# Kernel tuning notes

Hardware: AMD Instinct MI355X
Metric: run time of the kernel (lower is better)

The kernel has to match this reference:

```python
import jax, jax.numpy as jnp
import numpy as np

N = 50000   # nodes
E = 800000  # edges per layer
D = 128     # feature dim
H = 256     # mlp hidden
O = 3       # output dim


def setup_inputs() -> dict:
    key = jax.random.key(0)
    ks = jax.random.split(key, 16)
    def lin(k, fan_out, fan_in):
        s = 1.0 / np.sqrt(fan_in)
        kw, kb = jax.random.split(k)
        return (jax.random.uniform(kw, (fan_out, fan_in), jnp.float32, -s, s),
                jax.random.uniform(kb, (fan_out,), jnp.float32, -s, s))
    x = jax.random.normal(ks[0], (N, D), jnp.float32)
    edge_idx0 = jax.random.randint(ks[1], (2, E), 0, N, dtype=jnp.int64)
    edge_idx1 = jax.random.randint(ks[2], (2, E), 0, N, dtype=jnp.int64)
    Wl1, bl1 = lin(ks[3], D, D)   # SAGE layer1: lin_l (aggregated neighbors, with bias)
    Wr1, _ = lin(ks[4], D, D)     # SAGE layer1: lin_r (root, no bias)
    Wl2, bl2 = lin(ks[5], D, D)
    Wr2, _ = lin(ks[6], D, D)
    Ws, bs = lin(ks[7], D, D)     # skip_fc
    W1, b1 = lin(ks[8], H, D)     # mlp hidden
    W2, b2 = lin(ks[9], O, H)     # mlp out
    return dict(x=x, edge_idx0=edge_idx0, edge_idx1=edge_idx1,
                Wl1=Wl1, bl1=bl1, Wr1=Wr1, Wl2=Wl2, bl2=bl2, Wr2=Wr2,
                Ws=Ws, bs=bs, W1=W1, b1=b1, W2=W2, b2=b2)


def _sage(x, ei, Wl, bl, Wr):
    # PyG SAGEConv with mean aggregation: out = lin_l(mean_j x_j) + lin_r(x_i)
    src, dst = ei[0], ei[1]
    agg = jax.ops.segment_sum(x[src], dst, num_segments=N)          # [N, D] gather-scatter
    cnt = jax.ops.segment_sum(jnp.ones((ei.shape[1],), x.dtype), dst, num_segments=N)
    agg = agg / jnp.maximum(cnt, 1.0)[:, None]
    return agg @ Wl.T + bl + x @ Wr.T


def reference(x, edge_idx0, edge_idx1, Wl1, bl1, Wr1, Wl2, bl2, Wr2,
              Ws, bs, W1, b1, W2, b2):
    inp = x
    h = _sage(x, edge_idx0, Wl1, bl1, Wr1)
    h = _sage(h, edge_idx1, Wl2, bl2, Wr2)
    h = h + (inp @ Ws.T + bs)            # skip connection
    h = jax.nn.relu(h @ W1.T + b1)       # MLP head
    return h @ W2.T + b2                  # [N, 3]
```

## Files before the change

kernel.cpp:

```cpp
#include <hip/hip_runtime.h>
#include <hip/hip_bf16.h>


#define DD 128
#define SB 8
#define CH 4096
typedef unsigned short u16;
typedef __attribute__((ext_vector_type(8))) short short8;
typedef __attribute__((ext_vector_type(4))) float f32x4;

__device__ inline u16 f2bf(float f) {
    __hip_bfloat16 h = __float2bfloat16(f);
    u16 u;
    __builtin_memcpy(&u, &h, 2);
    return u;
}
__device__ inline unsigned pack2(float lo, float hi) {
    return (unsigned)f2bf(lo) | ((unsigned)f2bf(hi) << 16);
}
__device__ inline float bf_lo(unsigned u) { union { unsigned x; float f; } c; c.x = u << 16; return c.f; }
__device__ inline float bf_hi(unsigned u) { union { unsigned x; float f; } c; c.x = u & 0xffff0000u; return c.f; }

struct CastJobs {
    const float4* src[6];
    uint2* dst[6];
    int qstart[7];
};
__global__ __launch_bounds__(256) void cast_kernel(CastJobs jb) {
    int q = blockIdx.x * 256 + threadIdx.x;
    if (q >= jb.qstart[6]) return;
    int i = 0;
#pragma unroll
    for (int k = 1; k < 6; ++k) if (q >= jb.qstart[k]) i = k;
    int local = q - jb.qstart[i];
    float4 v = jb.src[i][local];
    jb.dst[i][local] = make_uint2(pack2(v.x, v.y), pack2(v.z, v.w));
}

__global__ __launch_bounds__(256) void hist1_kernel(const int* __restrict__ dst0, int* __restrict__ h0,
                                                    const int* __restrict__ dst1, int* __restrict__ h1,
                                                    int e0, int e1, int nb, int P) {
    int arr = blockIdx.y;
    const int* dst = arr ? dst1 : dst0;
    int* hist = arr ? h1 : h0;
    int e = arr ? e1 : e0;
    __shared__ int h[256];
    int t = threadIdx.x;
    h[t] = 0;
    __syncthreads();
    int base = blockIdx.x * CH;
    int hi = min(base + CH, e);
    for (int i = base + t; i < hi; i += 256) atomicAdd(&h[dst[i] >> SB], 1);
    __syncthreads();
    if (t < nb) hist[t * P + blockIdx.x] = h[t];
}

__global__ __launch_bounds__(256) void bscan_kernel(const int* __restrict__ h0, int* __restrict__ bb0, int* __restrict__ rp0, int e0,
                                                    const int* __restrict__ h1, int* __restrict__ bb1, int* __restrict__ rp1, int e1,
                                                    int nb, int P, int n) {
    int arr = blockIdx.x;
    const int* hist = arr ? h1 : h0;
    int* bb = arr ? bb1 : bb0;
    int* rp = arr ? rp1 : rp0;
    int E = arr ? e1 : e0;
    __shared__ int s[256];
    int t = threadIdx.x;
    int v = 0;
    if (t < nb) {
        const int* row = hist + (size_t)t * P;
        for (int p = 0; p < P; ++p) v += row[p];
    }
    s[t] = v;
    __syncthreads();
    for (int off = 1; off < 256; off <<= 1) {
        int u = (t >= off) ? s[t - off] : 0;
        __syncthreads();
        s[t] += u;
        __syncthreads();
    }
    if (t < nb) bb[t] = s[t] - v;
    if (t == 0) { bb[nb] = E; rp[n] = E; }
}

__global__ __launch_bounds__(256) void offs_kernel(int* __restrict__ h0, const int* __restrict__ bb0,
                                                   int* __restrict__ h1, const int* __restrict__ bb1,
                                                   int P) {
    int arr = blockIdx.y;
    int* hist = arr ? h1 : h0;
    const int* bb = arr ? bb1 : bb0;
    int b = blockIdx.x;
    __shared__ int s[256];
    int t = threadIdx.x;
    int v = (t < P) ? hist[b * P + t] : 0;
    s[t] = v;
    __syncthreads();
    for (int off = 1; off < 256; off <<= 1) {
        int u = (t >= off) ? s[t - off] : 0;
        __syncthreads();
        s[t] += u;
        __syncthreads();
    }
    if (t < P) hist[b * P + t] = s[t] - v + bb[b];
}

__global__ __launch_bounds__(256) void scatter1_kernel(
    const int* __restrict__ src0, const int* __restrict__ dst0, const int* __restrict__ h0, unsigned* __restrict__ binned0,
    const int* __restrict__ src1, const int* __restrict__ dst1, const int* __restrict__ h1, unsigned* __restrict__ binned1,
    int e0, int e1, int nb, int P) {
    int arr = blockIdx.y;
    const int* src = arr ? src1 : src0;
    const int* dst = arr ? dst1 : dst0;
    const int* hist = arr ? h1 : h0;
    unsigned* binned = arr ? binned1 : binned0;
    int e = arr ? e1 : e0;
    int p = blockIdx.x;
    __shared__ int cnt[256];
    int t = threadIdx.x;
    if (t < nb) cnt[t] = hist[t * P + p];
    __syncthreads();
    int base = p * CH;
    int hi = min(base + CH, e);
    for (int i = base + t; i < hi; i += 256) {
        int d = dst[i];
        int pos = atomicAdd(&cnt[d >> SB], 1);
        binned[pos] = ((unsigned)d << 16) | (unsigned)src[i];
    }
}

__global__ __launch_bounds__(256) void place_kernel(
    const unsigned* __restrict__ binned0, const int* __restrict__ bb0, int* __restrict__ rp0, u16* __restrict__ csr0,
    const unsigned* __restrict__ binned1, const int* __restrict__ bb1, int* __restrict__ rp1, u16* __restrict__ csr1,
    int n, int nb) {
    int arr = blockIdx.y;
    const unsigned* binned = arr ? binned1 : binned0;
    const int* bb = arr ? bb1 : bb0;
    int* rp = arr ? rp1 : rp0;
    u16* csr = arr ? csr1 : csr0;
    int b = blockIdx.x;
    __shared__ int cnt[256];
    __shared__ int s[256];
    int t = threadIdx.x;
    int base = bb[b], end = bb[b + 1];
    cnt[t] = 0;
    __syncthreads();
    for (int i = base + t; i < end; i += 256)
        atomicAdd(&cnt[(binned[i] >> 16) & 255], 1);
    __syncthreads();
    int deg = cnt[t];
    s[t] = deg;
    __syncthreads();
    for (int off = 1; off < 256; off <<= 1) {
        int u = (t >= off) ? s[t - off] : 0;
        __syncthreads();
        s[t] += u;
        __syncthreads();
    }
    int gpos = base + s[t] - deg;
    int node = (b << SB) + t;
    if (node < n) rp[node] = gpos;
    cnt[t] = gpos;
    __syncthreads();
    for (int i = base + t; i < end; i += 256) {
        unsigned pk = binned[i];
        int ld = (pk >> 16) & 255;
        int pos = atomicAdd(&cnt[ld], 1);
        csr[pos] = (u16)(pk & 0xffffu);
    }
}

__global__ __launch_bounds__(256) void agg1_kernel(const u16* __restrict__ G1,
                                                   const u16* __restrict__ csr,
                                                   const int* __restrict__ rp,
                                                   const float* __restrict__ bl1,
                                                   u16* __restrict__ h1, int n) {
    int g = (blockIdx.x * 256 + threadIdx.x) >> 4;
    int lane = threadIdx.x & 15;
    if (g >= n) return;
    int start = rp[g], end = rp[g + 1];
    int d = end - start;
    const uint4* X4 = (const uint4*)G1;
    float acc[8] = {0.f, 0.f, 0.f, 0.f, 0.f, 0.f, 0.f, 0.f};
    int e = start;
    for (; e + 1 < end; e += 2) {
        int s0 = csr[e], s1 = csr[e + 1];
        uint4 v0 = X4[(size_t)s0 * 48 + lane];
        uint4 v1 = X4[(size_t)s1 * 48 + lane];
        acc[0] += bf_lo(v0.x) + bf_lo(v1.x); acc[1] += bf_hi(v0.x) + bf_hi(v1.x);
        acc[2] += bf_lo(v0.y) + bf_lo(v1.y); acc[3] += bf_hi(v0.y) + bf_hi(v1.y);
        acc[4] += bf_lo(v0.z) + bf_lo(v1.z); acc[5] += bf_hi(v0.z) + bf_hi(v1.z);
        acc[6] += bf_lo(v0.w) + bf_lo(v1.w); acc[7] += bf_hi(v0.w) + bf_hi(v1.w);
    }
    if (e < end) {
        int s0 = csr[e];
        uint4 v0 = X4[(size_t)s0 * 48 + lane];
        acc[0] += bf_lo(v0.x); acc[1] += bf_hi(v0.x);
        acc[2] += bf_lo(v0.y); acc[3] += bf_hi(v0.y);
        acc[4] += bf_lo(v0.z); acc[5] += bf_hi(v0.z);
        acc[6] += bf_lo(v0.w); acc[7] += bf_hi(v0.w);
    }
    float sc = 1.0f / (float)max(d, 1);
    uint4 m = X4[(size_t)g * 48 + 16 + lane];
    const float4* bl = (const float4*)bl1;
    float4 ba = bl[lane * 2], bb = bl[lane * 2 + 1];
    uint4 r;
    r.x = pack2(acc[0] * sc + bf_lo(m.x) + ba.x, acc[1] * sc + bf_hi(m.x) + ba.y);
    r.y = pack2(acc[2] * sc + bf_lo(m.y) + ba.z, acc[3] * sc + bf_hi(m.y) + ba.w);
    r.z = pack2(acc[4] * sc + bf_lo(m.z) + bb.x, acc[5] * sc + bf_hi(m.z) + bb.y);
    r.w = pack2(acc[6] * sc + bf_lo(m.w) + bb.z, acc[7] * sc + bf_hi(m.w) + bb.w);
    ((uint4*)h1)[(size_t)g * 16 + lane] = r;
}

__global__ __launch_bounds__(256) void agg2_kernel(const u16* __restrict__ G2,
                                                   const u16* __restrict__ G1,
                                                   const u16* __restrict__ csr,
                                                   const int* __restrict__ rp,
                                                   const float* __restrict__ bl2,
                                                   const float* __restrict__ bs,
                                                   u16* __restrict__ h3, int n) {
    int g = (blockIdx.x * 256 + threadIdx.x) >> 4;
    int lane = threadIdx.x & 15;
    if (g >= n) return;
    int start = rp[g], end = rp[g + 1];
    int d = end - start;
    const uint4* X4 = (const uint4*)G2;
    float acc[8] = {0.f, 0.f, 0.f, 0.f, 0.f, 0.f, 0.f, 0.f};
    int e = start;
    for (; e + 1 < end; e += 2) {
        int s0 = csr[e], s1 = csr[e + 1];
        uint4 v0 = X4[(size_t)s0 * 32 + lane];
        uint4 v1 = X4[(size_t)s1 * 32 + lane];
        acc[0] += bf_lo(v0.x) + bf_lo(v1.x); acc[1] += bf_hi(v0.x) + bf_hi(v1.x);
        acc[2] += bf_lo(v0.y) + bf_lo(v1.y); acc[3] += bf_hi(v0.y) + bf_hi(v1.y);
        acc[4] += bf_lo(v0.z) + bf_lo(v1.z); acc[5] += bf_hi(v0.z) + bf_hi(v1.z);
        acc[6] += bf_lo(v0.w) + bf_lo(v1.w); acc[7] += bf_hi(v0.w) + bf_hi(v1.w);
    }
    if (e < end) {
        int s0 = csr[e];
        uint4 v0 = X4[(size_t)s0 * 32 + lane];
        acc[0] += bf_lo(v0.x); acc[1] += bf_hi(v0.x);
        acc[2] += bf_lo(v0.y); acc[3] += bf_hi(v0.y);
        acc[4] += bf_lo(v0.z); acc[5] += bf_hi(v0.z);
        acc[6] += bf_lo(v0.w); acc[7] += bf_hi(v0.w);
    }
    float sc = 1.0f / (float)max(d, 1);
    uint4 m2 = X4[(size_t)g * 32 + 16 + lane];
    uint4 m1 = ((const uint4*)G1)[(size_t)g * 48 + 32 + lane];
    const float4* c2 = (const float4*)bl2;
    const float4* cs = (const float4*)bs;
    float4 ba = c2[lane * 2], bb = c2[lane * 2 + 1];
    float4 sa = cs[lane * 2], sb = cs[lane * 2 + 1];
    uint4 r;
    r.x = pack2(acc[0] * sc + bf_lo(m2.x) + bf_lo(m1.x) + ba.x + sa.x,
                acc[1] * sc + bf_hi(m2.x) + bf_hi(m1.x) + ba.y + sa.y);
    r.y = pack2(acc[2] * sc + bf_lo(m2.y) + bf_lo(m1.y) + ba.z + sa.z,
                acc[3] * sc + bf_hi(m2.y) + bf_hi(m1.y) + ba.w + sa.w);
    r.z = pack2(acc[4] * sc + bf_lo(m2.z) + bf_lo(m1.z) + bb.x + sb.x,
                acc[5] * sc + bf_hi(m2.z) + bf_hi(m1.z) + bb.y + sb.y);
    r.w = pack2(acc[6] * sc + bf_lo(m2.w) + bf_lo(m1.w) + bb.z + sb.z,
                acc[7] * sc + bf_hi(m2.w) + bf_hi(m1.w) + bb.w + sb.w);
    ((uint4*)h3)[(size_t)g * 16 + lane] = r;
}

template <bool F32A>
__global__ __launch_bounds__(256) void mfma_gemm(const void* __restrict__ Av,
                                                 const u16* __restrict__ W,
                                                 const float* __restrict__ bias,
                                                 u16* __restrict__ C, int M, int NC, int mB) {
    __shared__ u16 As[64 * 136];
    __shared__ u16 Bs[128 * 136];
    const int t = threadIdx.x;
    const int rowBase = (blockIdx.x % mB) * 64;
    const int colBase = (blockIdx.x / mB) * 128;
    const int w = t >> 6, lane = t & 63, r = lane & 15, half = lane >> 4;

    f32x4 acc[8];
#pragma unroll
    for (int i = 0; i < 8; ++i) acc[i] = (f32x4){0.f, 0.f, 0.f, 0.f};

#pragma unroll
    for (int i = 0; i < 4; ++i) {
        int id = t + 256 * i, row = id >> 4, cc = id & 15;
        int gr = rowBase + row;
        uint4 v = make_uint4(0u, 0u, 0u, 0u);
        if (gr < M) {
            if (F32A) {
                const float* A = (const float*)Av;
                float4 a = *(const float4*)&A[(size_t)gr * DD + cc * 8];
                float4 b = *(const float4*)&A[(size_t)gr * DD + cc * 8 + 4];
                v = make_uint4(pack2(a.x, a.y), pack2(a.z, a.w), pack2(b.x, b.y), pack2(b.z, b.w));
            } else {
                v = ((const uint4*)Av)[(size_t)gr * 16 + cc];
            }
        }
        *(uint4*)&As[row * 136 + cc * 8] = v;
    }
#pragma unroll
    for (int i = 0; i < 8; ++i) {
        int id = t + 256 * i, row = id >> 4, cc = id & 15;
        *(uint4*)&Bs[row * 136 + cc * 8] = ((const uint4*)W)[(size_t)(colBase + row) * 16 + cc];
    }
    __syncthreads();
    const u16* aB = &As[(w * 16 + r) * 136 + half * 8];
    const u16* bB = &Bs[r * 136 + half * 8];
#pragma unroll
    for (int kk = 0; kk < 4; ++kk) {
        short8 af = *(const short8*)(aB + kk * 32);
#pragma unroll
        for (int ct = 0; ct < 8; ++ct) {
            short8 bf = *(const short8*)(bB + ct * (16 * 136) + kk * 32);
            acc[ct] = __builtin_amdgcn_mfma_f32_16x16x32_bf16(af, bf, acc[ct], 0, 0, 0);
        }
    }

#pragma unroll
    for (int ct = 0; ct < 8; ++ct) {
        int col = colBase + ct * 16 + r;
        float bv = bias ? bias[col] : 0.f;
#pragma unroll
        for (int reg = 0; reg < 4; ++reg) {
            int row = rowBase + w * 16 + half * 4 + reg;
            if (row < M) C[(size_t)row * NC + col] = f2bf(acc[ct][reg] + bv);
        }
    }
}

__global__ __launch_bounds__(256) void gemm_out_kernel(const u16* __restrict__ h3,
                                                       const u16* __restrict__ W1,
                                                       const float* __restrict__ b1,
                                                       const float* __restrict__ W2,
                                                       const float* __restrict__ b2,
                                                       float* __restrict__ out, int M) {
    __shared__ u16 As[64 * 136];
    __shared__ u16 Bs[128 * 136];
    __shared__ float w2s[3 * 256];
    __shared__ float b1s[256];
    const int t = threadIdx.x;
    const int rowBase = blockIdx.x * 64;
    const int w = t >> 6, lane = t & 63, r = lane & 15, half = lane >> 4;

    for (int i = t; i < 768; i += 256) w2s[i] = W2[i];
    b1s[t] = b1[t];
#pragma unroll
    for (int i = 0; i < 4; ++i) {
        int id = t + 256 * i, row = id >> 4, cc = id & 15;
        int gr = rowBase + row;
        uint4 v = make_uint4(0u, 0u, 0u, 0u);
        if (gr < M) v = ((const uint4*)h3)[(size_t)gr * 16 + cc];
        *(uint4*)&As[row * 136 + cc * 8] = v;
    }

    f32x4 acc[2][8];
#pragma unroll
    for (int ch = 0; ch < 2; ++ch)
#pragma unroll
        for (int i = 0; i < 8; ++i) acc[ch][i] = (f32x4){0.f, 0.f, 0.f, 0.f};

    for (int ch = 0; ch < 2; ++ch) {
        __syncthreads();
        if (ch) {
        }
#pragma unroll
        for (int i = 0; i < 8; ++i) {
            int id = t + 256 * i, row = id >> 4, cc = id & 15;
            *(uint4*)&Bs[row * 136 + cc * 8] = ((const uint4*)W1)[(size_t)(ch * 128 + row) * 16 + cc];
        }
        __syncthreads();
        const u16* aB = &As[(w * 16 + r) * 136 + half * 8];
        const u16* bB = &Bs[r * 136 + half * 8];
#pragma unroll
        for (int kk = 0; kk < 4; ++kk) {
            short8 af = *(const short8*)(aB + kk * 32);
#pragma unroll
            for (int ct = 0; ct < 8; ++ct) {
                short8 bf = *(const short8*)(bB + ct * (16 * 136) + kk * 32);
                acc[ch][ct] = __builtin_amdgcn_mfma_f32_16x16x32_bf16(af, bf, acc[ch][ct], 0, 0, 0);
            }
        }
    }

    float p[4][3] = {{0.f}};
#pragma unroll
    for (int ch = 0; ch < 2; ++ch) {
#pragma unroll
        for (int ct = 0; ct < 8; ++ct) {
            int col = ch * 128 + ct * 16 + r;
            float bv = b1s[col];
            float w0 = w2s[0 * 256 + col], w1 = w2s[1 * 256 + col], w2v = w2s[2 * 256 + col];
#pragma unroll
            for (int reg = 0; reg < 4; ++reg) {
                float h4 = fmaxf(acc[ch][ct][reg] + bv, 0.f);
                p[reg][0] += h4 * w0;
                p[reg][1] += h4 * w1;
                p[reg][2] += h4 * w2v;
            }
        }
    }
#pragma unroll
    for (int m = 1; m < 16; m <<= 1)
#pragma unroll
        for (int reg = 0; reg < 4; ++reg)
#pragma unroll
            for (int o = 0; o < 3; ++o) p[reg][o] += __shfl_xor(p[reg][o], m);
    if (r == 0) {
#pragma unroll
        for (int reg = 0; reg < 4; ++reg) {
            int row = rowBase + w * 16 + half * 4 + reg;
            if (row < M) {
                out[(size_t)row * 3 + 0] = p[reg][0] + b2[0];
                out[(size_t)row * 3 + 1] = p[reg][1] + b2[1];
                out[(size_t)row * 3 + 2] = p[reg][2] + b2[2];
            }
        }
    }
}

extern "C" void kernel_launch(void* const* d_in, const int* in_sizes, int n_in,
                              void* d_out, int out_size, void* d_ws, size_t ws_size,
                              hipStream_t stream) {
    const float* x   = (const float*)d_in[0];
    const int*   ei0 = (const int*)d_in[1];
    const int*   ei1 = (const int*)d_in[2];
    const float* Wl1 = (const float*)d_in[3];
    const float* bl1 = (const float*)d_in[4];
    const float* Wr1 = (const float*)d_in[5];
    const float* Wl2 = (const float*)d_in[6];
    const float* bl2 = (const float*)d_in[7];
    const float* Wr2 = (const float*)d_in[8];
    const float* Wsk = (const float*)d_in[9];
    const float* bsk = (const float*)d_in[10];
    const float* W1  = (const float*)d_in[11];
    const float* b1  = (const float*)d_in[12];
    const float* W2  = (const float*)d_in[13];
    const float* b2  = (const float*)d_in[14];
    float* out = (float*)d_out;

    const int N  = in_sizes[0] / DD;
    const int E0 = in_sizes[1] / 2;
    const int E1 = in_sizes[2] / 2;
    const int H  = in_sizes[12];

    const int* src0 = ei0;      const int* dst0 = ei0 + E0;
    const int* src1 = ei1;      const int* dst1 = ei1 + E1;

    const int nb   = (N + 255) >> SB;
    const int Emax = (E0 > E1) ? E0 : E1;
    const int P    = (Emax + CH - 1) / CH;

    char* wp = (char*)d_ws;
    auto carve = [&](size_t bytes) { char* p = wp; wp += (bytes + 255) & ~(size_t)255; return p; };
    u16* G1   = (u16*)carve((size_t)N * 384 * 2);
    u16* G2   = (u16*)carve((size_t)N * 256 * 2);
    u16* h1h  = (u16*)carve((size_t)N * DD * 2);
    u16* h3h  = (u16*)carve((size_t)N * DD * 2);
    u16* wc1  = (u16*)carve((size_t)384 * DD * 2);
    u16* wc2  = (u16*)carve((size_t)256 * DD * 2);
    u16* w1h  = (u16*)carve((size_t)H * DD * 2);
    int* rp0  = (int*)carve((size_t)(N + 1) * 4);
    int* rp1  = (int*)carve((size_t)(N + 1) * 4);
    u16* csr0 = (u16*)carve((size_t)E0 * 2);
    u16* csr1 = (u16*)carve((size_t)E1 * 2);
    unsigned* binned0 = (unsigned*)carve((size_t)E0 * 4);
    unsigned* binned1 = (unsigned*)carve((size_t)E1 * 4);
    int* hist1_0 = (int*)carve((size_t)nb * P * 4);
    int* hist1_1 = (int*)carve((size_t)nb * P * 4);
    int* bb0 = (int*)carve((size_t)(nb + 1) * 4);
    int* bb1 = (int*)carve((size_t)(nb + 1) * 4);

    CastJobs jb;
    const float* srcs[6] = {Wl1, Wr1, Wsk, Wl2, Wr2, W1};
    u16* dsts[6] = {wc1, wc1 + 128 * DD, wc1 + 256 * DD, wc2, wc2 + 128 * DD, w1h};
    int  cnts[6] = {DD * DD, DD * DD, DD * DD, DD * DD, DD * DD, H * DD};
    int q = 0;
    for (int i = 0; i < 6; ++i) {
        jb.src[i] = (const float4*)srcs[i];
        jb.dst[i] = (uint2*)dsts[i];
        jb.qstart[i] = q;
        q += cnts[i] / 4;
    }
    jb.qstart[6] = q;

    const int gAgg = (N * 16 + 255) / 256;
    const int mB   = (N + 63) / 64;

    cast_kernel<<<(q + 255) / 256, 256, 0, stream>>>(jb);
    hist1_kernel<<<dim3(P, 2), 256, 0, stream>>>(dst0, hist1_0, dst1, hist1_1, E0, E1, nb, P);
    bscan_kernel<<<2, 256, 0, stream>>>(hist1_0, bb0, rp0, E0, hist1_1, bb1, rp1, E1, nb, P, N);
    offs_kernel<<<dim3(nb, 2), 256, 0, stream>>>(hist1_0, bb0, hist1_1, bb1, P);
    scatter1_kernel<<<dim3(P, 2), 256, 0, stream>>>(src0, dst0, hist1_0, binned0,
                                                    src1, dst1, hist1_1, binned1, E0, E1, nb, P);
    place_kernel<<<dim3(nb, 2), 256, 0, stream>>>(binned0, bb0, rp0, csr0,
                                                  binned1, bb1, rp1, csr1, N, nb);

    mfma_gemm<true><<<mB * 3, 256, 0, stream>>>(x, wc1, nullptr, G1, N, 384, mB);
    agg1_kernel<<<gAgg, 256, 0, stream>>>(G1, csr0, rp0, bl1, h1h, N);
    mfma_gemm<false><<<mB * 2, 256, 0, stream>>>(h1h, wc2, nullptr, G2, N, 256, mB);
    agg2_kernel<<<gAgg, 256, 0, stream>>>(G2, G1, csr1, rp1, bl2, bsk, h3h, N);
    gemm_out_kernel<<<mB, 256, 0, stream>>>(h3h, w1h, b1, W2, b2, out, N);
}
```

Before: 294.2 us.

## Persistent MFMA GEMMs with preswizzled weights, parallel histogram rowsum, deeper gather unroll

The GEMMs become persistent kernels. Each block loads its weight slice once into LDS in an MFMA-friendly swizzled layout, and each wave loops over 16-row tiles, reading A directly from global memory into registers instead of staging it through LDS. The output GEMM keeps all 256 hidden columns in registers per tile, which removes its two-chunk reload. The single-block serial histogram row sum is split into a parallel rowsum kernel, and the aggregation loops unroll to four gathers per step for more memory-level parallelism. The code assumes M is divisible by 16 since bounds checks were dropped, and it uses more registers.

```diff
diff --git a/kernel.cpp b/kernel.cpp
--- a/kernel.cpp
+++ b/kernel.cpp
@@ -55,21 +55,35 @@
     if (t < nb) hist[t * P + blockIdx.x] = h[t];
 }
 
-__global__ __launch_bounds__(256) void bscan_kernel(const int* __restrict__ h0, int* __restrict__ bb0, int* __restrict__ rp0, int e0,
-                                                    const int* __restrict__ h1, int* __restrict__ bb1, int* __restrict__ rp1, int e1,
-                                                    int nb, int P, int n) {
+__global__ __launch_bounds__(256) void rowsum_kernel(const int* __restrict__ h0, int* __restrict__ bs0,
+                                                     const int* __restrict__ h1, int* __restrict__ bs1,
+                                                     int P) {
+    int arr = blockIdx.y;
+    const int* hist = arr ? h1 : h0;
+    int* bs = arr ? bs1 : bs0;
+    int b = blockIdx.x;
+    __shared__ int s[256];
+    int t = threadIdx.x;
+    s[t] = (t < P) ? hist[b * P + t] : 0;
+    __syncthreads();
+    for (int off = 128; off; off >>= 1) {
+        if (t < off) s[t] += s[t + off];
+        __syncthreads();
+    }
+    if (t == 0) bs[b] = s[0];
+}
+
+__global__ __launch_bounds__(256) void bscan_kernel(const int* __restrict__ bs0, int* __restrict__ bb0, int* __restrict__ rp0, int e0,
+                                                    const int* __restrict__ bs1, int* __restrict__ bb1, int* __restrict__ rp1, int e1,
+                                                    int nb, int n) {
     int arr = blockIdx.x;
-    const int* hist = arr ? h1 : h0;
+    const int* bsum = arr ? bs1 : bs0;
     int* bb = arr ? bb1 : bb0;
     int* rp = arr ? rp1 : rp0;
     int E = arr ? e1 : e0;
     __shared__ int s[256];
     int t = threadIdx.x;
-    int v = 0;
-    if (t < nb) {
-        const int* row = hist + (size_t)t * P;
-        for (int p = 0; p < P; ++p) v += row[p];
-    }
+    int v = (t < nb) ? bsum[t] : 0;
     s[t] = v;
     __syncthreads();
     for (int off = 1; off < 256; off <<= 1) {
@@ -181,18 +195,23 @@
     const uint4* X4 = (const uint4*)G1;
     float acc[8] = {0.f, 0.f, 0.f, 0.f, 0.f, 0.f, 0.f, 0.f};
     int e = start;
-    for (; e + 1 < end; e += 2) {
-        int s0 = csr[e], s1 = csr[e + 1];
+    for (; e + 3 < end; e += 4) {
+        int s0 = csr[e], s1 = csr[e + 1], s2 = csr[e + 2], s3 = csr[e + 3];
         uint4 v0 = X4[(size_t)s0 * 48 + lane];
         uint4 v1 = X4[(size_t)s1 * 48 + lane];
-        acc[0] += bf_lo(v0.x) + bf_lo(v1.x); acc[1] += bf_hi(v0.x) + bf_hi(v1.x);
-        acc[2] += bf_lo(v0.y) + bf_lo(v1.y); acc[3] += bf_hi(v0.y) + bf_hi(v1.y);
-        acc[4] += bf_lo(v0.z) + bf_lo(v1.z); acc[5] += bf_hi(v0.z) + bf_hi(v1.z);
-        acc[6] += bf_lo(v0.w) + bf_lo(v1.w); acc[7] += bf_hi(v0.w) + bf_hi(v1.w);
-    }
-    if (e < end) {
-        int s0 = csr[e];
-        uint4 v0 = X4[(size_t)s0 * 48 + lane];
+        uint4 v2 = X4[(size_t)s2 * 48 + lane];
+        uint4 v3 = X4[(size_t)s3 * 48 + lane];
+        acc[0] += (bf_lo(v0.x) + bf_lo(v1.x)) + (bf_lo(v2.x) + bf_lo(v3.x));
+        acc[1] += (bf_hi(v0.x) + bf_hi(v1.x)) + (bf_hi(v2.x) + bf_hi(v3.x));
+        acc[2] += (bf_lo(v0.y) + bf_lo(v1.y)) + (bf_lo(v2.y) + bf_lo(v3.y));
+        acc[3] += (bf_hi(v0.y) + bf_hi(v1.y)) + (bf_hi(v2.y) + bf_hi(v3.y));
+        acc[4] += (bf_lo(v0.z) + bf_lo(v1.z)) + (bf_lo(v2.z) + bf_lo(v3.z));
+        acc[5] += (bf_hi(v0.z) + bf_hi(v1.z)) + (bf_hi(v2.z) + bf_hi(v3.z));
+        acc[6] += (bf_lo(v0.w) + bf_lo(v1.w)) + (bf_lo(v2.w) + bf_lo(v3.w));
+        acc[7] += (bf_hi(v0.w) + bf_hi(v1.w)) + (bf_hi(v2.w) + bf_hi(v3.w));
+    }
+    for (; e < end; ++e) {
+        uint4 v0 = X4[(size_t)csr[e] * 48 + lane];
         acc[0] += bf_lo(v0.x); acc[1] += bf_hi(v0.x);
         acc[2] += bf_lo(v0.y); acc[3] += bf_hi(v0.y);
         acc[4] += bf_lo(v0.z); acc[5] += bf_hi(v0.z);
@@ -225,18 +244,23 @@
     const uint4* X4 = (const uint4*)G2;
     float acc[8] = {0.f, 0.f, 0.f, 0.f, 0.f, 0.f, 0.f, 0.f};
     int e = start;
-    for (; e + 1 < end; e += 2) {
-        int s0 = csr[e], s1 = csr[e + 1];
+    for (; e + 3 < end; e += 4) {
+        int s0 = csr[e], s1 = csr[e + 1], s2 = csr[e + 2], s3 = csr[e + 3];
         uint4 v0 = X4[(size_t)s0 * 32 + lane];
         uint4 v1 = X4[(size_t)s1 * 32 + lane];
-        acc[0] += bf_lo(v0.x) + bf_lo(v1.x); acc[1] += bf_hi(v0.x) + bf_hi(v1.x);
-        acc[2] += bf_lo(v0.y) + bf_lo(v1.y); acc[3] += bf_hi(v0.y) + bf_hi(v1.y);
-        acc[4] += bf_lo(v0.z) + bf_lo(v1.z); acc[5] += bf_hi(v0.z) + bf_hi(v1.z);
-        acc[6] += bf_lo(v0.w) + bf_lo(v1.w); acc[7] += bf_hi(v0.w) + bf_hi(v1.w);
-    }
-    if (e < end) {
-        int s0 = csr[e];
-        uint4 v0 = X4[(size_t)s0 * 32 + lane];
+        uint4 v2 = X4[(size_t)s2 * 32 + lane];
+        uint4 v3 = X4[(size_t)s3 * 32 + lane];
+        acc[0] += (bf_lo(v0.x) + bf_lo(v1.x)) + (bf_lo(v2.x) + bf_lo(v3.x));
+        acc[1] += (bf_hi(v0.x) + bf_hi(v1.x)) + (bf_hi(v2.x) + bf_hi(v3.x));
+        acc[2] += (bf_lo(v0.y) + bf_lo(v1.y)) + (bf_lo(v2.y) + bf_lo(v3.y));
+        acc[3] += (bf_hi(v0.y) + bf_hi(v1.y)) + (bf_hi(v2.y) + bf_hi(v3.y));
+        acc[4] += (bf_lo(v0.z) + bf_lo(v1.z)) + (bf_lo(v2.z) + bf_lo(v3.z));
+        acc[5] += (bf_hi(v0.z) + bf_hi(v1.z)) + (bf_hi(v2.z) + bf_hi(v3.z));
+        acc[6] += (bf_lo(v0.w) + bf_lo(v1.w)) + (bf_lo(v2.w) + bf_lo(v3.w));
+        acc[7] += (bf_hi(v0.w) + bf_hi(v1.w)) + (bf_hi(v2.w) + bf_hi(v3.w));
+    }
+    for (; e < end; ++e) {
+        uint4 v0 = X4[(size_t)csr[e] * 32 + lane];
         acc[0] += bf_lo(v0.x); acc[1] += bf_hi(v0.x);
         acc[2] += bf_lo(v0.y); acc[3] += bf_hi(v0.y);
         acc[4] += bf_lo(v0.z); acc[5] += bf_hi(v0.z);
@@ -264,62 +288,61 @@
 template <bool F32A>
 __global__ __launch_bounds__(256) void mfma_gemm(const void* __restrict__ Av,
                                                  const u16* __restrict__ W,
-                                                 const float* __restrict__ bias,
-                                                 u16* __restrict__ C, int M, int NC, int mB) {
-    __shared__ u16 As[64 * 136];
-    __shared__ u16 Bs[128 * 136];
+                                                 u16* __restrict__ C, int M, int NC) {
+    __shared__ u16 Bs[32 * 512];
     const int t = threadIdx.x;
-    const int rowBase = (blockIdx.x % mB) * 64;
-    const int colBase = (blockIdx.x / mB) * 128;
+    const int colBase = blockIdx.y * 128;
+#pragma unroll
+    for (int i = 0; i < 8; ++i) {
+        int id = t + 256 * i;
+        int nrow = id >> 4, cc = id & 15;
+        int f = ((nrow >> 4) << 2) | (cc >> 2);
+        int dl = ((cc & 3) << 4) | (nrow & 15);
+        *(uint4*)&Bs[(f * 64 + dl) * 8] = ((const uint4*)W)[(size_t)(colBase + nrow) * 16 + cc];
+    }
+    __syncthreads();
     const int w = t >> 6, lane = t & 63, r = lane & 15, half = lane >> 4;
-
-    f32x4 acc[8];
-#pragma unroll
-    for (int i = 0; i < 8; ++i) acc[i] = (f32x4){0.f, 0.f, 0.f, 0.f};
-
-#pragma unroll
-    for (int i = 0; i < 4; ++i) {
-        int id = t + 256 * i, row = id >> 4, cc = id & 15;
-        int gr = rowBase + row;
-        uint4 v = make_uint4(0u, 0u, 0u, 0u);
-        if (gr < M) {
-            if (F32A) {
-                const float* A = (const float*)Av;
-                float4 a = *(const float4*)&A[(size_t)gr * DD + cc * 8];
-                float4 b = *(const float4*)&A[(size_t)gr * DD + cc * 8 + 4];
-                v = make_uint4(pack2(a.x, a.y), pack2(a.z, a.w), pack2(b.x, b.y), pack2(b.z, b.w));
-            } else {
-                v = ((const uint4*)Av)[(size_t)gr * 16 + cc];
+    const int nTiles = M >> 4;
+    const int nWaves = gridDim.x * 4;
+    const u16* bB = &Bs[lane * 8];
+    for (int tile = blockIdx.x * 4 + w; tile < nTiles; tile += nWaves) {
+        int rowA = (tile << 4) + r;
+        short8 af[4];
+        if (F32A) {
+            const float4* Arow = (const float4*)Av + (size_t)rowA * 32 + half * 2;
+#pragma unroll
+            for (int kk = 0; kk < 4; ++kk) {
+                float4 a = Arow[kk * 8], b = Arow[kk * 8 + 1];
+                uint4 v = make_uint4(pack2(a.x, a.y), pack2(a.z, a.w),
+                                     pack2(b.x, b.y), pack2(b.z, b.w));
+                af[kk] = *(short8*)&v;
+            }
+        } else {
+            const uint4* Arow = (const uint4*)Av + (size_t)rowA * 16 + half;
+#pragma unroll
+            for (int kk = 0; kk < 4; ++kk) {
+                uint4 v = Arow[kk * 4];
+                af[kk] = *(short8*)&v;
             }
         }
-        *(uint4*)&As[row * 136 + cc * 8] = v;
-    }
-#pragma unroll
-    for (int i = 0; i < 8; ++i) {
-        int id = t + 256 * i, row = id >> 4, cc = id & 15;
-        *(uint4*)&Bs[row * 136 + cc * 8] = ((const uint4*)W)[(size_t)(colBase + row) * 16 + cc];
-    }
-    __syncthreads();
-    const u16* aB = &As[(w * 16 + r) * 136 + half * 8];
-    const u16* bB = &Bs[r * 136 + half * 8];
-#pragma unroll
-    for (int kk = 0; kk < 4; ++kk) {
-        short8 af = *(const short8*)(aB + kk * 32);
+        f32x4 acc[8];
+#pragma unroll
+        for (int i = 0; i < 8; ++i) acc[i] = (f32x4){0.f, 0.f, 0.f, 0.f};
+#pragma unroll
+        for (int kk = 0; kk < 4; ++kk)
+#pragma unroll
+            for (int ct = 0; ct < 8; ++ct) {
+                short8 bf = *(const short8*)(bB + (ct * 4 + kk) * 512);
+                acc[ct] = __builtin_amdgcn_mfma_f32_16x16x32_bf16(af[kk], bf, acc[ct], 0, 0, 0);
+            }
 #pragma unroll
         for (int ct = 0; ct < 8; ++ct) {
-            short8 bf = *(const short8*)(bB + ct * (16 * 136) + kk * 32);
-            acc[ct] = __builtin_amdgcn_mfma_f32_16x16x32_bf16(af, bf, acc[ct], 0, 0, 0);
-        }
-    }
-
-#pragma unroll
-    for (int ct = 0; ct < 8; ++ct) {
-        int col = colBase + ct * 16 + r;
-        float bv = bias ? bias[col] : 0.f;
-#pragma unroll
-        for (int reg = 0; reg < 4; ++reg) {
-            int row = rowBase + w * 16 + half * 4 + reg;
-            if (row < M) C[(size_t)row * NC + col] = f2bf(acc[ct][reg] + bv);
+            int col = colBase + ct * 16 + r;
+#pragma unroll
+            for (int reg = 0; reg < 4; ++reg) {
+                int row = (tile << 4) + half * 4 + reg;
+                C[(size_t)row * NC + col] = f2bf(acc[ct][reg]);
+            }
         }
     }
 }
@@ -330,85 +353,74 @@
                                                        const float* __restrict__ W2,
                                                        const float* __restrict__ b2,
                                                        float* __restrict__ out, int M) {
-    __shared__ u16 As[64 * 136];
-    __shared__ u16 Bs[128 * 136];
+    __shared__ u16 Bs[64 * 512];
     __shared__ float w2s[3 * 256];
     __shared__ float b1s[256];
     const int t = threadIdx.x;
-    const int rowBase = blockIdx.x * 64;
-    const int w = t >> 6, lane = t & 63, r = lane & 15, half = lane >> 4;
-
+#pragma unroll
+    for (int i = 0; i < 16; ++i) {
+        int id = t + 256 * i;
+        int nrow = id >> 4, cc = id & 15;
+        int f = ((nrow >> 4) << 2) | (cc >> 2);
+        int dl = ((cc & 3) << 4) | (nrow & 15);
+        *(uint4*)&Bs[(f * 64 + dl) * 8] = ((const uint4*)W1)[(size_t)nrow * 16 + cc];
+    }
     for (int i = t; i < 768; i += 256) w2s[i] = W2[i];
     b1s[t] = b1[t];
-#pragma unroll
-    for (int i = 0; i < 4; ++i) {
-        int id = t + 256 * i, row = id >> 4, cc = id & 15;
-        int gr = rowBase + row;
-        uint4 v = make_uint4(0u, 0u, 0u, 0u);
-        if (gr < M) v = ((const uint4*)h3)[(size_t)gr * 16 + cc];
-        *(uint4*)&As[row * 136 + cc * 8] = v;
-    }
-
-    f32x4 acc[2][8];
-#pragma unroll
-    for (int ch = 0; ch < 2; ++ch)
-#pragma unroll
-        for (int i = 0; i < 8; ++i) acc[ch][i] = (f32x4){0.f, 0.f, 0.f, 0.f};
-
-    for (int ch = 0; ch < 2; ++ch) {
-        __syncthreads();
-        if (ch) {
+    __syncthreads();
+    const int w = t >> 6, lane = t & 63, r = lane & 15, half = lane >> 4;
+    const int nTiles = M >> 4;
+    const int nWaves = gridDim.x * 4;
+    const u16* bB = &Bs[lane * 8];
+    float c0 = b2[0], c1 = b2[1], c2 = b2[2];
+    for (int tile = blockIdx.x * 4 + w; tile < nTiles; tile += nWaves) {
+        int rowA = (tile << 4) + r;
+        const uint4* Arow = (const uint4*)h3 + (size_t)rowA * 16 + half;
+        short8 af[4];
+#pragma unroll
+        for (int kk = 0; kk < 4; ++kk) {
+            uint4 v = Arow[kk * 4];
+            af[kk] = *(short8*)&v;
         }
-#pragma unroll
-        for (int i = 0; i < 8; ++i) {
-            int id = t + 256 * i, row = id >> 4, cc = id & 15;
-            *(uint4*)&Bs[row * 136 + cc * 8] = ((const uint4*)W1)[(size_t)(ch * 128 + row) * 16 + cc];
-        }
-        __syncthreads();
-        const u16* aB = &As[(w * 16 + r) * 136 + half * 8];
-        const u16* bB = &Bs[r * 136 + half * 8];
-#pragma unroll
-        for (int kk = 0; kk < 4; ++kk) {
-            short8 af = *(const short8*)(aB + kk * 32);
-#pragma unroll
-            for (int ct = 0; ct < 8; ++ct) {
-                short8 bf = *(const short8*)(bB + ct * (16 * 136) + kk * 32);
-                acc[ch][ct] = __builtin_amdgcn_mfma_f32_16x16x32_bf16(af, bf, acc[ch][ct], 0, 0, 0);
-            }
-        }
-    }
-
-    float p[4][3] = {{0.f}};
-#pragma unroll
-    for (int ch = 0; ch < 2; ++ch) {
-#pragma unroll
-        for (int ct = 0; ct < 8; ++ct) {
-            int col = ch * 128 + ct * 16 + r;
+        f32x4 acc[16];
+#pragma unroll
+        for (int i = 0; i < 16; ++i) acc[i] = (f32x4){0.f, 0.f, 0.f, 0.f};
+#pragma unroll
+        for (int kk = 0; kk < 4; ++kk)
+#pragma unroll
+            for (int ct = 0; ct < 16; ++ct) {
+                short8 bf = *(const short8*)(bB + (ct * 4 + kk) * 512);
+                acc[ct] = __builtin_amdgcn_mfma_f32_16x16x32_bf16(af[kk], bf, acc[ct], 0, 0, 0);
+            }
+        float p[4][3] = {{0.f, 0.f, 0.f}, {0.f, 0.f, 0.f}, {0.f, 0.f, 0.f}, {0.f, 0.f, 0.f}};
+#pragma unroll
+        for (int ct = 0; ct < 16; ++ct) {
+            int col = ct * 16 + r;
             float bv = b1s[col];
-            float w0 = w2s[0 * 256 + col], w1 = w2s[1 * 256 + col], w2v = w2s[2 * 256 + col];
+            float w0 = w2s[col], w1 = w2s[256 + col], w2v = w2s[512 + col];
 #pragma unroll
             for (int reg = 0; reg < 4; ++reg) {
-                float h4 = fmaxf(acc[ch][ct][reg] + bv, 0.f);
+                float h4 = fmaxf(acc[ct][reg] + bv, 0.f);
                 p[reg][0] += h4 * w0;
                 p[reg][1] += h4 * w1;
                 p[reg][2] += h4 * w2v;
             }
         }
-    }
-#pragma unroll
-    for (int m = 1; m < 16; m <<= 1)
-#pragma unroll
-        for (int reg = 0; reg < 4; ++reg)
-#pragma unroll
-            for (int o = 0; o < 3; ++o) p[reg][o] += __shfl_xor(p[reg][o], m);
-    if (r == 0) {
-#pragma unroll
-        for (int reg = 0; reg < 4; ++reg) {
-            int row = rowBase + w * 16 + half * 4 + reg;
-            if (row < M) {
-                out[(size_t)row * 3 + 0] = p[reg][0] + b2[0];
-                out[(size_t)row * 3 + 1] = p[reg][1] + b2[1];
-                out[(size_t)row * 3 + 2] = p[reg][2] + b2[2];
+#pragma unroll
+        for (int m = 1; m < 16; m <<= 1)
+#pragma unroll
+            for (int reg = 0; reg < 4; ++reg) {
+                p[reg][0] += __shfl_xor(p[reg][0], m);
+                p[reg][1] += __shfl_xor(p[reg][1], m);
+                p[reg][2] += __shfl_xor(p[reg][2], m);
+            }
+        if (r == 0) {
+#pragma unroll
+            for (int reg = 0; reg < 4; ++reg) {
+                int row = (tile << 4) + half * 4 + reg;
+                out[(size_t)row * 3 + 0] = p[reg][0] + c0;
+                out[(size_t)row * 3 + 1] = p[reg][1] + c1;
+                out[(size_t)row * 3 + 2] = p[reg][2] + c2;
             }
         }
     }
@@ -463,6 +475,8 @@
     unsigned* binned1 = (unsigned*)carve((size_t)E1 * 4);
     int* hist1_0 = (int*)carve((size_t)nb * P * 4);
     int* hist1_1 = (int*)carve((size_t)nb * P * 4);
+    int* bsum0 = (int*)carve((size_t)nb * 4);
+    int* bsum1 = (int*)carve((size_t)nb * 4);
     int* bb0 = (int*)carve((size_t)(nb + 1) * 4);
     int* bb1 = (int*)carve((size_t)(nb + 1) * 4);
 
@@ -480,20 +494,20 @@
     jb.qstart[6] = q;
 
     const int gAgg = (N * 16 + 255) / 256;
-    const int mB   = (N + 63) / 64;
 
     cast_kernel<<<(q + 255) / 256, 256, 0, stream>>>(jb);
     hist1_kernel<<<dim3(P, 2), 256, 0, stream>>>(dst0, hist1_0, dst1, hist1_1, E0, E1, nb, P);
-    bscan_kernel<<<2, 256, 0, stream>>>(hist1_0, bb0, rp0, E0, hist1_1, bb1, rp1, E1, nb, P, N);
+    rowsum_kernel<<<dim3(nb, 2), 256, 0, stream>>>(hist1_0, bsum0, hist1_1, bsum1, P);
+    bscan_kernel<<<2, 256, 0, stream>>>(bsum0, bb0, rp0, E0, bsum1, bb1, rp1, E1, nb, N);
     offs_kernel<<<dim3(nb, 2), 256, 0, stream>>>(hist1_0, bb0, hist1_1, bb1, P);
     scatter1_kernel<<<dim3(P, 2), 256, 0, stream>>>(src0, dst0, hist1_0, binned0,
                                                     src1, dst1, hist1_1, binned1, E0, E1, nb, P);
     place_kernel<<<dim3(nb, 2), 256, 0, stream>>>(binned0, bb0, rp0, csr0,
                                                   binned1, bb1, rp1, csr1, N, nb);
 
-    mfma_gemm<true><<<mB * 3, 256, 0, stream>>>(x, wc1, nullptr, G1, N, 384, mB);
+    mfma_gemm<true><<<dim3(320, 3), 256, 0, stream>>>(x, wc1, G1, N, 384);
     agg1_kernel<<<gAgg, 256, 0, stream>>>(G1, csr0, rp0, bl1, h1h, N);
-    mfma_gemm<false><<<mB * 2, 256, 0, stream>>>(h1h, wc2, nullptr, G2, N, 256, mB);
+    mfma_gemm<false><<<dim3(320, 2), 256, 0, stream>>>(h1h, wc2, G2, N, 256);
     agg2_kernel<<<gAgg, 256, 0, stream>>>(G2, G1, csr1, rp1, bl2, bsk, h3h, N);
-    gemm_out_kernel<<<mB, 256, 0, stream>>>(h3h, w1h, b1, W2, b2, out, N);
-}
+    gemm_out_kernel<<<512, 256, 0, stream>>>(h3h, w1h, b1, W2, b2, out, N);
+}
```

New measurement: 257.6 us. 12.4% less time.
